# Kernel tuning notes

Measured on AMD Instinct MI355X. Metric: run time of the kernel, lower is better.

## Reference

```python
import jax, jax.numpy as jnp
import numpy as np

NUM_HEADS = 12
THRESHOLD = 0.005

def setup_inputs() -> dict:
    key = jax.random.key(0)
    ks = jax.random.split(key, 7)
    B, N, C = 8, 1024, 768
    return {
        "x": jax.random.normal(ks[0], (B, N, C), jnp.float32),
        "qkv_weight": jax.random.normal(ks[1], (3 * C, C), jnp.float32) * 0.02,
        "qkv_bias": jax.random.normal(ks[2], (3 * C,), jnp.float32) * 0.02,
        "proj_weight": jax.random.normal(ks[3], (C, C), jnp.float32) * 0.02,
        "proj_bias": jax.random.normal(ks[4], (C,), jnp.float32) * 0.02,
        "mask_real": jax.random.uniform(ks[5], (3 * C, C), jnp.float32),
        "mask_real_proj": jax.random.uniform(ks[6], (C, C), jnp.float32),
    }

def _binarize(m, thr):
    # Binarizer.forward: 1 where m >= thr else 0
    return (m >= thr).astype(m.dtype)

def reference(x, qkv_weight, qkv_bias, proj_weight, proj_bias, mask_real, mask_real_proj):
    B, N, C = x.shape
    H = NUM_HEADS
    D = C // H
    scale = D ** -0.5
    qkv_w = qkv_weight * _binarize(mask_real, THRESHOLD)
    proj_w = proj_weight * _binarize(mask_real_proj, THRESHOLD)
    # qkv projection: [B,N,3C]
    qkv = jnp.einsum('bnc,oc->bno', x, qkv_w) + qkv_bias
    qkv = qkv.reshape(B, N, 3, H, D).transpose(2, 0, 3, 1, 4)  # [3,B,H,N,D]
    q, k, v = qkv[0], qkv[1], qkv[2]
    attn = jnp.einsum('bhnd,bhmd->bhnm', q, k) * scale
    attn = jax.nn.softmax(attn, axis=-1)
    out = jnp.einsum('bhnm,bhmd->bhnd', attn, v)  # [B,H,N,D]
    out = out.transpose(0, 2, 1, 3).reshape(B, N, C)
    out = jnp.einsum('bnc,oc->bno', out, proj_w) + proj_bias
    return out
```

## Files before the change

### kernel.cpp

```cpp
#include <hip/hip_runtime.h>
#include <hip/hip_bf16.h>

typedef short bf16x8 __attribute__((ext_vector_type(8)));
typedef float f32x4 __attribute__((ext_vector_type(4)));

typedef __attribute__((address_space(3))) unsigned int lds_u32;
typedef __attribute__((address_space(1))) const unsigned int gbl_cu32;

__device__ __forceinline__ void async_ld16(void* lds, const void* g) {
  __builtin_amdgcn_global_load_lds((gbl_cu32*)g, (lds_u32*)lds, 16, 0, 0);
}

__device__ __forceinline__ unsigned short f2bf(float f) {
  unsigned u = __builtin_bit_cast(unsigned, f);
  u += 0x7FFFu + ((u >> 16) & 1u);
  return (unsigned short)(u >> 16);
}

__global__ void k_prep(const float* __restrict__ x, unsigned short* __restrict__ xo,
                       const float* __restrict__ w1, const float* __restrict__ m1,
                       unsigned short* __restrict__ o1,
                       const float* __restrict__ w2, const float* __restrict__ m2,
                       unsigned short* __restrict__ o2) {
  int blk = blockIdx.x;
  if (blk < 6144) {
    int i = blk * 256 + threadIdx.x;
    float4 v = ((const float4*)x)[i];
    ushort4 r;
    r.x = f2bf(v.x); r.y = f2bf(v.y); r.z = f2bf(v.z); r.w = f2bf(v.w);
    ((ushort4*)xo)[i] = r;
  } else if (blk < 6144 + 1728) {
    int i = (blk - 6144) * 256 + threadIdx.x;
    float4 wv = ((const float4*)w1)[i];
    float4 mv = ((const float4*)m1)[i];
    ushort4 r;
    r.x = f2bf(mv.x >= 0.005f ? wv.x : 0.0f);
    r.y = f2bf(mv.y >= 0.005f ? wv.y : 0.0f);
    r.z = f2bf(mv.z >= 0.005f ? wv.z : 0.0f);
    r.w = f2bf(mv.w >= 0.005f ? wv.w : 0.0f);
    ((ushort4*)o1)[i] = r;
  } else {
    int i = (blk - 6144 - 1728) * 256 + threadIdx.x;
    float4 wv = ((const float4*)w2)[i];
    float4 mv = ((const float4*)m2)[i];
    ushort4 r;
    r.x = f2bf(mv.x >= 0.005f ? wv.x : 0.0f);
    r.y = f2bf(mv.y >= 0.005f ? wv.y : 0.0f);
    r.z = f2bf(mv.z >= 0.005f ? wv.z : 0.0f);
    r.w = f2bf(mv.w >= 0.005f ? wv.w : 0.0f);
    ((ushort4*)o2)[i] = r;
  }
}

template <bool OUT_BF16>
__global__ __launch_bounds__(256) void k_gemm_bt(
    const unsigned short* __restrict__ A,
    const unsigned short* __restrict__ Bw,
    const float* __restrict__ bias,
    void* __restrict__ Cout,
    int M, int Nn, int K)
{
  __shared__ unsigned short As[128 * 64];
  __shared__ unsigned short Bs[128 * 64];
  const int tid = threadIdx.x, lane = tid & 63;
  const int wv = tid >> 6, wr = wv >> 1, wc = wv & 1;
  const int q4 = lane >> 4, r = lane & 15;
  const long bm = (long)blockIdx.x * 128, bn = (long)blockIdx.y * 128;

  f32x4 acc[4][4] = {};

  int srow[4], sco[4];
#pragma unroll
  for (int j = 0; j < 4; ++j) {
    const int s = j * 256 + tid;
    srow[j] = s >> 3;
    sco[j] = ((s & 7) ^ (srow[j] & 7)) * 16;
  }

  for (int k0 = 0; k0 < K; k0 += 64) {
    __syncthreads();
#pragma unroll
    for (int j = 0; j < 4; ++j) {
      const int ldsoff = j * 4096 + tid * 16;
      async_ld16((char*)As + ldsoff,
                 (const char*)(A + (bm + srow[j]) * (long)K + k0) + sco[j]);
      async_ld16((char*)Bs + ldsoff,
                 (const char*)(Bw + (bn + srow[j]) * (long)K + k0) + sco[j]);
    }
    __syncthreads();

#pragma unroll
    for (int ks = 0; ks < 2; ++ks) {
      bf16x8 af[4], bfr[4];
#pragma unroll
      for (int i = 0; i < 4; ++i) {
        const int row = wr * 64 + i * 16 + r;
        const int ch = (ks * 4 + q4) ^ (row & 7);
        af[i] = *(const bf16x8*)(As + row * 64 + ch * 8);
      }
#pragma unroll
      for (int j = 0; j < 4; ++j) {
        const int row = wc * 64 + j * 16 + r;
        const int ch = (ks * 4 + q4) ^ (row & 7);
        bfr[j] = *(const bf16x8*)(Bs + row * 64 + ch * 8);
      }
#pragma unroll
      for (int i = 0; i < 4; ++i)
#pragma unroll
        for (int j = 0; j < 4; ++j)
          acc[i][j] = __builtin_amdgcn_mfma_f32_16x16x32_bf16(af[i], bfr[j], acc[i][j], 0, 0, 0);
    }
  }

#pragma unroll
  for (int j = 0; j < 4; ++j) {
    const long col = bn + wc * 64 + j * 16 + r;
    const float bv = bias[col];
#pragma unroll
    for (int i = 0; i < 4; ++i) {
#pragma unroll
      for (int rr = 0; rr < 4; ++rr) {
        const long rowg = bm + wr * 64 + i * 16 + q4 * 4 + rr;
        const float v = acc[i][j][rr] + bv;
        if (OUT_BF16)
          ((unsigned short*)Cout)[rowg * Nn + col] = f2bf(v);
        else
          ((float*)Cout)[rowg * Nn + col] = v;
      }
    }
  }
}

__global__ __launch_bounds__(256) void k_transpose_v(const unsigned short* __restrict__ qkv,
                                                     unsigned short* __restrict__ vt) {
  __shared__ unsigned short T[64][72];
  const int tid = threadIdx.x;
  const int bh = blockIdx.y, b = bh / 12, h = bh % 12;
  const int n0 = blockIdx.x * 64;
#pragma unroll
  for (int i = 0; i < 2; ++i) {
    int c = tid + i * 256, row = c >> 3, ch = c & 7;
    uint4 v = *(const uint4*)(qkv + ((long)(b * 1024 + n0 + row)) * 2304 + 1536 + h * 64 + ch * 8);
    *(uint4*)(&T[row][ch * 8]) = v;
  }
  __syncthreads();
#pragma unroll
  for (int i = 0; i < 2; ++i) {
    int c = tid + i * 256, d = c >> 3, ch = c & 7;
    unsigned short tmp[8];
#pragma unroll
    for (int j = 0; j < 8; ++j) tmp[j] = T[ch * 8 + j][d];
    *(uint4*)(vt + ((long)bh * 64 + d) * 1024 + n0 + ch * 8) = *(const uint4*)tmp;
  }
}

__global__ __launch_bounds__(256) void k_flash(
    const unsigned short* __restrict__ qkv,
    const unsigned short* __restrict__ vt,
    unsigned short* __restrict__ outp)
{
  constexpr int LD = 72;
  __shared__ unsigned short Ks[64 * LD];
  __shared__ unsigned short Vts[64 * LD];
  __shared__ unsigned short Ps[4 * 32 * LD];

  const int tid = threadIdx.x, lane = tid & 63;
  const int wv = tid >> 6, q4 = lane >> 4, r = lane & 15;
  const int bh = blockIdx.y, b = bh / 12, h = bh % 12;
  const int q0 = blockIdx.x * 128;
  const long qrow0 = (long)b * 1024;

  bf16x8 aq[2][2];
#pragma unroll
  for (int i = 0; i < 2; ++i)
#pragma unroll
    for (int kc = 0; kc < 2; ++kc)
      aq[i][kc] = *(const bf16x8*)(qkv + (qrow0 + q0 + wv * 32 + i * 16 + r) * 2304 + h * 64 + kc * 32 + q4 * 8);

  f32x4 o[2][4] = {};
  f32x4 lsum[2] = {};
  const bf16x8 ones = {0x3F80, 0x3F80, 0x3F80, 0x3F80, 0x3F80, 0x3F80, 0x3F80, 0x3F80};

  for (int kt = 0; kt < 16; ++kt) {
    const int n0 = kt * 64;
    __syncthreads();
#pragma unroll
    for (int i = 0; i < 2; ++i) {
      int c = tid + i * 256, row = c >> 3, ch = c & 7;
      uint4 kv = *(const uint4*)(qkv + (qrow0 + n0 + row) * 2304 + 768 + h * 64 + ch * 8);
      *(uint4*)(Ks + row * LD + ch * 8) = kv;
      uint4 vvv = *(const uint4*)(vt + ((long)bh * 64 + row) * 1024 + n0 + ch * 8);
      *(uint4*)(Vts + row * LD + ch * 8) = vvv;
    }
    __syncthreads();

    f32x4 s[2][4] = {};
    {
      bf16x8 bk[4][2];
#pragma unroll
      for (int j = 0; j < 4; ++j)
#pragma unroll
        for (int kc = 0; kc < 2; ++kc)
          bk[j][kc] = *(const bf16x8*)(Ks + (j * 16 + r) * LD + kc * 32 + q4 * 8);
#pragma unroll
      for (int i = 0; i < 2; ++i)
#pragma unroll
        for (int j = 0; j < 4; ++j) {
          s[i][j] = __builtin_amdgcn_mfma_f32_16x16x32_bf16(aq[i][0], bk[j][0], s[i][j], 0, 0, 0);
          s[i][j] = __builtin_amdgcn_mfma_f32_16x16x32_bf16(aq[i][1], bk[j][1], s[i][j], 0, 0, 0);
        }
    }

#pragma unroll
    for (int i = 0; i < 2; ++i)
#pragma unroll
      for (int j = 0; j < 4; ++j)
#pragma unroll
        for (int rr = 0; rr < 4; ++rr) {
          float p = __expf(fmaf(s[i][j][rr], 0.125f, -2.0f));
          Ps[(wv * 32 + i * 16 + q4 * 4 + rr) * LD + j * 16 + r] = f2bf(p);
        }

    {
      bf16x8 bv[4][2];
#pragma unroll
      for (int jd = 0; jd < 4; ++jd)
#pragma unroll
        for (int kc = 0; kc < 2; ++kc)
          bv[jd][kc] = *(const bf16x8*)(Vts + (jd * 16 + r) * LD + kc * 32 + q4 * 8);
#pragma unroll
      for (int i = 0; i < 2; ++i) {
        bf16x8 ap0 = *(const bf16x8*)(Ps + (wv * 32 + i * 16 + r) * LD + 0 + q4 * 8);
        bf16x8 ap1 = *(const bf16x8*)(Ps + (wv * 32 + i * 16 + r) * LD + 32 + q4 * 8);
        lsum[i] = __builtin_amdgcn_mfma_f32_16x16x32_bf16(ap0, ones, lsum[i], 0, 0, 0);
        lsum[i] = __builtin_amdgcn_mfma_f32_16x16x32_bf16(ap1, ones, lsum[i], 0, 0, 0);
#pragma unroll
        for (int jd = 0; jd < 4; ++jd) {
          o[i][jd] = __builtin_amdgcn_mfma_f32_16x16x32_bf16(ap0, bv[jd][0], o[i][jd], 0, 0, 0);
          o[i][jd] = __builtin_amdgcn_mfma_f32_16x16x32_bf16(ap1, bv[jd][1], o[i][jd], 0, 0, 0);
        }
      }
    }
  }

#pragma unroll
  for (int i = 0; i < 2; ++i)
#pragma unroll
    for (int rr = 0; rr < 4; ++rr) {
      const float inv = 1.0f / lsum[i][rr];
      const long rowg = qrow0 + q0 + wv * 32 + i * 16 + q4 * 4 + rr;
#pragma unroll
      for (int jd = 0; jd < 4; ++jd)
        outp[rowg * 768 + h * 64 + jd * 16 + r] = f2bf(o[i][jd][rr] * inv);
    }
}

extern "C" void kernel_launch(void* const* d_in, const int* in_sizes, int n_in,
                              void* d_out, int out_size, void* d_ws, size_t ws_size,
                              hipStream_t stream) {
  const float* x      = (const float*)d_in[0];
  const float* qkv_w  = (const float*)d_in[1];
  const float* qkv_b  = (const float*)d_in[2];
  const float* proj_w = (const float*)d_in[3];
  const float* proj_b = (const float*)d_in[4];
  const float* mask   = (const float*)d_in[5];
  const float* mask_p = (const float*)d_in[6];

  char* ws = (char*)d_ws;
  unsigned short* qkv   = (unsigned short*)(ws);
  unsigned short* vt    = (unsigned short*)(ws + 37748736);
  unsigned short* xbf   = (unsigned short*)(ws + 50331648);
  unsigned short* wqkv  = (unsigned short*)(ws + 62914560);
  unsigned short* wproj = (unsigned short*)(ws + 66453504);

  k_prep<<<8448, 256, 0, stream>>>(x, xbf, qkv_w, mask, wqkv, proj_w, mask_p, wproj);
  k_gemm_bt<true><<<dim3(64, 18), 256, 0, stream>>>(xbf, wqkv, qkv_b, qkv, 8192, 2304, 768);
  k_transpose_v<<<dim3(16, 96), 256, 0, stream>>>(qkv, vt);
  k_flash<<<dim3(8, 96), 256, 0, stream>>>(qkv, vt, xbf);
  k_gemm_bt<false><<<dim3(64, 6), 256, 0, stream>>>(xbf, wproj, proj_b, d_out, 8192, 768, 768);
}
```

Measured before the change: 225.1 us.

## Double-buffer K/V tiles with async global-to-LDS loads and XOR swizzle

The flash attention kernel now fetches K and V^T tiles directly into LDS with async global_load_lds into two ping-pong buffers. Each iteration issues the next tile's load right after the barrier, so the fetch overlaps with the current tile's MFMA work, and one barrier per iteration is removed. The padded LDS rows are replaced by an unpadded 64-wide layout with an XOR chunk swizzle to avoid bank conflicts. This doubles K/V LDS usage, which may lower occupancy. Correctness relies on the barrier waiting for outstanding async loads.

```diff
diff --git a/kernel.cpp b/kernel.cpp
--- a/kernel.cpp
+++ b/kernel.cpp
@@ -159,10 +159,10 @@
     const unsigned short* __restrict__ vt,
     unsigned short* __restrict__ outp)
 {
-  constexpr int LD = 72;
-  __shared__ unsigned short Ks[64 * LD];
-  __shared__ unsigned short Vts[64 * LD];
-  __shared__ unsigned short Ps[4 * 32 * LD];
+  constexpr int LDP = 72;
+  __shared__ unsigned short Ks[2][64 * 64];
+  __shared__ unsigned short Vts[2][64 * 64];
+  __shared__ unsigned short Ps[4 * 32 * LDP];
 
   const int tid = threadIdx.x, lane = tid & 63;
   const int wv = tid >> 6, q4 = lane >> 4, r = lane & 15;
@@ -170,6 +170,17 @@
   const int q0 = blockIdx.x * 128;
   const long qrow0 = (long)b * 1024;
 
+  int srow[2], sco[2];
+#pragma unroll
+  for (int i = 0; i < 2; ++i) {
+    const int s = i * 256 + tid;
+    srow[i] = s >> 3;
+    sco[i] = ((s & 7) ^ (srow[i] & 7)) * 8;
+  }
+
+  const unsigned short* Kg = qkv + qrow0 * 2304 + 768 + (long)h * 64;
+  const unsigned short* Vg = vt + (long)bh * 64 * 1024;
+
   bf16x8 aq[2][2];
 #pragma unroll
   for (int i = 0; i < 2; ++i)
@@ -181,18 +192,26 @@
   f32x4 lsum[2] = {};
   const bf16x8 ones = {0x3F80, 0x3F80, 0x3F80, 0x3F80, 0x3F80, 0x3F80, 0x3F80, 0x3F80};
 
+  auto stage = [&](int n0, int buf) {
+#pragma unroll
+    for (int i = 0; i < 2; ++i) {
+      const int ldsoff = (i * 256 + tid) * 16;
+      async_ld16((char*)Ks[buf] + ldsoff,
+                 (const void*)(Kg + (long)(n0 + srow[i]) * 2304 + sco[i]));
+      async_ld16((char*)Vts[buf] + ldsoff,
+                 (const void*)(Vg + (long)srow[i] * 1024 + n0 + sco[i]));
+    }
+  };
+
+  stage(0, 0);
+
   for (int kt = 0; kt < 16; ++kt) {
-    const int n0 = kt * 64;
+    const int cur = kt & 1;
     __syncthreads();
-#pragma unroll
-    for (int i = 0; i < 2; ++i) {
-      int c = tid + i * 256, row = c >> 3, ch = c & 7;
-      uint4 kv = *(const uint4*)(qkv + (qrow0 + n0 + row) * 2304 + 768 + h * 64 + ch * 8);
-      *(uint4*)(Ks + row * LD + ch * 8) = kv;
-      uint4 vvv = *(const uint4*)(vt + ((long)bh * 64 + row) * 1024 + n0 + ch * 8);
-      *(uint4*)(Vts + row * LD + ch * 8) = vvv;
-    }
-    __syncthreads();
+    if (kt < 15) stage((kt + 1) * 64, cur ^ 1);
+
+    const unsigned short* Kc = Ks[cur];
+    const unsigned short* Vc = Vts[cur];
 
     f32x4 s[2][4] = {};
     {
@@ -200,8 +219,11 @@
 #pragma unroll
       for (int j = 0; j < 4; ++j)
 #pragma unroll
-        for (int kc = 0; kc < 2; ++kc)
-          bk[j][kc] = *(const bf16x8*)(Ks + (j * 16 + r) * LD + kc * 32 + q4 * 8);
+        for (int kc = 0; kc < 2; ++kc) {
+          const int row = j * 16 + r;
+          const int ch = (kc * 4 + q4) ^ (row & 7);
+          bk[j][kc] = *(const bf16x8*)(Kc + row * 64 + ch * 8);
+        }
 #pragma unroll
       for (int i = 0; i < 2; ++i)
 #pragma unroll
@@ -218,7 +240,7 @@
 #pragma unroll
         for (int rr = 0; rr < 4; ++rr) {
           float p = __expf(fmaf(s[i][j][rr], 0.125f, -2.0f));
-          Ps[(wv * 32 + i * 16 + q4 * 4 + rr) * LD + j * 16 + r] = f2bf(p);
+          Ps[(wv * 32 + i * 16 + q4 * 4 + rr) * LDP + j * 16 + r] = f2bf(p);
         }
 
     {
@@ -226,12 +248,15 @@
 #pragma unroll
       for (int jd = 0; jd < 4; ++jd)
 #pragma unroll
-        for (int kc = 0; kc < 2; ++kc)
-          bv[jd][kc] = *(const bf16x8*)(Vts + (jd * 16 + r) * LD + kc * 32 + q4 * 8);
+        for (int kc = 0; kc < 2; ++kc) {
+          const int row = jd * 16 + r;
+          const int ch = (kc * 4 + q4) ^ (row & 7);
+          bv[jd][kc] = *(const bf16x8*)(Vc + row * 64 + ch * 8);
+        }
 #pragma unroll
       for (int i = 0; i < 2; ++i) {
-        bf16x8 ap0 = *(const bf16x8*)(Ps + (wv * 32 + i * 16 + r) * LD + 0 + q4 * 8);
-        bf16x8 ap1 = *(const bf16x8*)(Ps + (wv * 32 + i * 16 + r) * LD + 32 + q4 * 8);
+        bf16x8 ap0 = *(const bf16x8*)(Ps + (wv * 32 + i * 16 + r) * LDP + 0 + q4 * 8);
+        bf16x8 ap1 = *(const bf16x8*)(Ps + (wv * 32 + i * 16 + r) * LDP + 32 + q4 * 8);
         lsum[i] = __builtin_amdgcn_mfma_f32_16x16x32_bf16(ap0, ones, lsum[i], 0, 0, 0);
         lsum[i] = __builtin_amdgcn_mfma_f32_16x16x32_bf16(ap1, ones, lsum[i], 0, 0, 0);
 #pragma unroll
```

After: 214.9 us. 1.05x faster.
